# Kernel tuning notes

Hardware: AMD Instinct MI355X
Metric: run time of the kernel (lower is better)

Reference implementation:

```python
import jax, jax.numpy as jnp
import numpy as np

EPS = 1e-7
MAX_TANH = 1.0 - 1e-6  # clamp for arctanh stability


def _norm(v):
    # last-axis L2 norm, clamped away from zero
    return jnp.maximum(jnp.linalg.norm(v, axis=-1, keepdims=True), EPS)


def log_map_zero(y):
    # Poincare ball (c=1) log map at the origin
    n = _norm(y)
    return jnp.arctanh(jnp.clip(n, 0.0, MAX_TANH)) * y / n


def exp_map_zero(v):
    # Poincare ball (c=1) exp map at the origin
    n = _norm(v)
    return jnp.tanh(n) * v / n


def h_add(x, y):
    # Mobius addition x (+) y on the Poincare ball (c=1)
    xy = jnp.sum(x * y, axis=-1, keepdims=True)
    x2 = jnp.sum(x * x, axis=-1, keepdims=True)
    y2 = jnp.sum(y * y, axis=-1, keepdims=True)
    num = (1.0 + 2.0 * xy + y2) * x + (1.0 - x2) * y
    den = 1.0 + 2.0 * xy + x2 * y2
    return num / jnp.maximum(den, EPS)


def h_mul(x, W):
    # Mobius matrix-vector multiply: exp0( log0(x) @ W )
    return exp_map_zero(log_map_zero(x) @ W)


def setup_inputs() -> dict:
    key = jax.random.key(0)
    k1, k2, k3, k4 = jax.random.split(key, 4)
    N, F_IN, F_OUT = 8192, 128, 128
    # node features inside the unit ball: ||x|| ~ 0.05*sqrt(128) ~ 0.57
    x = 0.05 * jax.random.normal(k1, (N, F_IN), dtype=jnp.float32)
    # sparse-ish row-normalized dense adjacency
    a = (jax.random.uniform(k2, (N, N)) < 0.01).astype(jnp.float32)
    adj = a / jnp.maximum(a.sum(axis=1, keepdims=True), 1.0)
    # xavier-uniform-ish weights
    lim_e = np.sqrt(6.0 / (F_IN + F_IN)) * np.sqrt(2.0)
    lim_l = np.sqrt(6.0 / (2 * F_IN + F_OUT)) * np.sqrt(2.0)
    embed = jax.random.uniform(k3, (F_IN, F_IN), minval=-lim_e, maxval=lim_e, dtype=jnp.float32)
    layer = jax.random.uniform(k4, (2 * F_IN, F_OUT), minval=-lim_l, maxval=lim_l, dtype=jnp.float32)
    embed_bias = jnp.zeros((F_IN,), dtype=jnp.float32)
    layer_bias = jnp.zeros((F_OUT,), dtype=jnp.float32)
    return {"x": x, "adj": adj, "embed": embed, "layer": layer,
            "embed_bias": embed_bias, "layer_bias": layer_bias}


def reference(x, adj, embed, layer, embed_bias, layer_bias):
    # h = (embed (x)mobius x) (+) embed_bias
    h = h_mul(x, embed)                      # [N, F_IN]
    h = h_add(h, embed_bias[None, :])
    # neighbor aggregation in tangent space at origin
    neigh = exp_map_zero(adj @ log_map_zero(h))   # [N, F_IN]
    # out = (layer (x)mobius [x ; neigh]) (+) layer_bias
    out = h_mul(jnp.concatenate((x, neigh), axis=1), layer)  # [N, F_OUT]
    out = h_add(out, layer_bias[None, :])
    return out
```

## Files before the change

### kernel.cpp

```cpp
#include <hip/hip_runtime.h>
#include <hip/hip_bf16.h>
#include <math.h>

#define EPS  1e-7f
#define MAXT 0.999999f

typedef short  s16x8  __attribute__((ext_vector_type(8)));
typedef float  f32x16 __attribute__((ext_vector_type(16)));
typedef float  f32x4  __attribute__((ext_vector_type(4)));

__device__ __forceinline__ float waveRedSum(float v) {
    #pragma unroll
    for (int off = 32; off > 0; off >>= 1)
        v += __shfl_xor(v, off, 64);
    return v;
}

__device__ __forceinline__ unsigned short f2bf(float f) {
    unsigned u = __float_as_uint(f);
    u += 0x7fff + ((u >> 16) & 1);
    return (unsigned short)(u >> 16);
}

__global__ __launch_bounds__(256) void kA(const float* __restrict__ x,
                                          const float* __restrict__ embed,
                                          const float* __restrict__ ebias,
                                          unsigned short* __restrict__ vpack) {
    __shared__ float u[4][128];
    const int wave = threadIdx.x >> 6;
    const int lane = threadIdx.x & 63;
    const int row  = blockIdx.x * 4 + wave;
    const int c0   = lane * 2;

    const float2 xr = *(const float2*)(x + (size_t)row * 128 + c0);

    float n2 = waveRedSum(xr.x * xr.x + xr.y * xr.y);
    float n  = fmaxf(sqrtf(n2), EPS);
    float sc = atanhf(fminf(n, MAXT)) / n;
    u[wave][c0]     = xr.x * sc;
    u[wave][c0 + 1] = xr.y * sc;
    __syncthreads();

    float a0 = 0.f, a1 = 0.f;
    #pragma unroll 8
    for (int k = 0; k < 128; k++) {
        float  uk = u[wave][k];
        float2 e  = *(const float2*)(embed + (size_t)k * 128 + c0);
        a0 = fmaf(uk, e.x, a0);
        a1 = fmaf(uk, e.y, a1);
    }

    float np2 = waveRedSum(a0 * a0 + a1 * a1);
    float np  = fmaxf(sqrtf(np2), EPS);
    float se  = tanhf(np) / np;
    float h0 = a0 * se, h1 = a1 * se;
    float x2 = np2 * se * se;

    float bx = ebias[c0], by = ebias[c0 + 1];
    float xy = waveRedSum(h0 * bx + h1 * by);
    float y2 = waveRedSum(bx * bx + by * by);
    float den = fmaxf(1.f + 2.f * xy + x2 * y2, EPS);
    float cx = 1.f + 2.f * xy + y2;
    float cy = 1.f - x2;
    float hb0 = (cx * h0 + cy * bx) / den;
    float hb1 = (cx * h1 + cy * by) / den;

    float m2 = waveRedSum(hb0 * hb0 + hb1 * hb1);
    float m  = fmaxf(sqrtf(m2), EPS);
    float sl = atanhf(fminf(m, MAXT)) / m;
    float v0 = hb0 * sl, v1 = hb1 * sl;

    const int tbase = (row >> 4) * 2048 + (row & 15);
    vpack[tbase + c0 * 16]       = f2bf(v0);
    vpack[tbase + (c0 + 1) * 16] = f2bf(v1);
}

__device__ __forceinline__ s16x8 pack_bf16x8(const f32x4 a, const f32x4 b) {
    union { __hip_bfloat162 h[4]; s16x8 v; } r;
    r.h[0] = __float22bfloat162_rn({a.x, a.y});
    r.h[1] = __float22bfloat162_rn({a.z, a.w});
    r.h[2] = __float22bfloat162_rn({b.x, b.y});
    r.h[3] = __float22bfloat162_rn({b.z, b.w});
    return r.v;
}

__global__ __launch_bounds__(256) void kB(const float* __restrict__ adj,
                                          const unsigned short* __restrict__ vpack,
                                          float* __restrict__ tpart,
                                          int klen) {
    const int wave = threadIdx.x >> 6;
    const int lane = threadIdx.x & 63;
    const int rt   = blockIdx.x * 4 + wave;
    const int r0   = rt * 32;
    const int k0   = blockIdx.y * klen;
    float* tout    = tpart + (size_t)blockIdx.y * (8192 * 128);

    const int m  = lane & 31;
    const int kh = lane >> 5;

    const float* abase = adj + (size_t)(r0 + m) * 8192 + k0 + kh * 8;
    const unsigned short* bbase = vpack + (size_t)(k0 >> 4) * 2048 + m * 16 + kh * 8;

    const int kiters = klen >> 4;

    f32x16 acc0 = {0.f}, acc1 = {0.f}, acc2 = {0.f}, acc3 = {0.f};

    f32x4 aq[4][2];
    s16x8 bq[2][4];

    #pragma unroll
    for (int c = 0; c < 4; ++c) {
        aq[c][0] = *(const f32x4*)(abase + c * 16);
        aq[c][1] = *(const f32x4*)(abase + c * 16 + 4);
    }
    #pragma unroll
    for (int c = 0; c < 2; ++c) {
        const unsigned short* bp = bbase + (size_t)c * 2048;
        bq[c][0] = *(const s16x8*)(bp);
        bq[c][1] = *(const s16x8*)(bp + 512);
        bq[c][2] = *(const s16x8*)(bp + 1024);
        bq[c][3] = *(const s16x8*)(bp + 1536);
    }

    for (int it = 0; it < kiters; it += 4) {
        #pragma unroll
        for (int u = 0; u < 4; ++u) {
            const int c = it + u;
            s16x8 af = pack_bf16x8(aq[u][0], aq[u][1]);
            acc0 = __builtin_amdgcn_mfma_f32_32x32x16_bf16(af, bq[u & 1][0], acc0, 0, 0, 0);
            acc1 = __builtin_amdgcn_mfma_f32_32x32x16_bf16(af, bq[u & 1][1], acc1, 0, 0, 0);
            acc2 = __builtin_amdgcn_mfma_f32_32x32x16_bf16(af, bq[u & 1][2], acc2, 0, 0, 0);
            acc3 = __builtin_amdgcn_mfma_f32_32x32x16_bf16(af, bq[u & 1][3], acc3, 0, 0, 0);

            {
                const int cb = min(c + 2, kiters - 1);
                const unsigned short* bp = bbase + (size_t)cb * 2048;
                bq[u & 1][0] = *(const s16x8*)(bp);
                bq[u & 1][1] = *(const s16x8*)(bp + 512);
                bq[u & 1][2] = *(const s16x8*)(bp + 1024);
                bq[u & 1][3] = *(const s16x8*)(bp + 1536);
            }
            {
                const int ca = min(c + 4, kiters - 1);
                aq[u][0] = *(const f32x4*)(abase + (size_t)ca * 16);
                aq[u][1] = *(const f32x4*)(abase + (size_t)ca * 16 + 4);
            }
        }
    }

    #pragma unroll
    for (int r = 0; r < 16; ++r) {
        int row  = r0 + (r & 3) + 8 * (r >> 2) + 4 * kh;
        float* o = tout + (size_t)row * 128 + m;
        o[0]  = acc0[r];
        o[32] = acc1[r];
        o[64] = acc2[r];
        o[96] = acc3[r];
    }
}

__global__ __launch_bounds__(256) void kC(const float* __restrict__ x,
                                          const float* __restrict__ tpart,
                                          const float* __restrict__ layer,
                                          const float* __restrict__ lbias,
                                          float* __restrict__ out,
                                          int S) {
    __shared__ float w[4][256];
    const int wave = threadIdx.x >> 6;
    const int lane = threadIdx.x & 63;
    const int row  = blockIdx.x * 4 + wave;
    const int c0   = lane * 2;

    float2 tr = *(const float2*)(tpart + (size_t)row * 128 + c0);
    for (int s = 1; s < S; s++) {
        float2 p = *(const float2*)(tpart + (size_t)s * 8192 * 128 + (size_t)row * 128 + c0);
        tr.x += p.x; tr.y += p.y;
    }
    const float2 xr = *(const float2*)(x + (size_t)row * 128 + c0);

    float st = waveRedSum(tr.x * tr.x + tr.y * tr.y);
    float sx = waveRedSum(xr.x * xr.x + xr.y * xr.y);

    float nt = fmaxf(sqrtf(st), EPS);
    float se = tanhf(nt) / nt;

    float ncat2 = sx + st * se * se;
    float ncat  = fmaxf(sqrtf(ncat2), EPS);
    float sw    = atanhf(fminf(ncat, MAXT)) / ncat;
    w[wave][c0]           = xr.x * sw;
    w[wave][c0 + 1]       = xr.y * sw;
    w[wave][128 + c0]     = tr.x * se * sw;
    w[wave][128 + c0 + 1] = tr.y * se * sw;
    __syncthreads();

    float a0 = 0.f, a1 = 0.f;
    #pragma unroll 8
    for (int k = 0; k < 256; k++) {
        float  wk = w[wave][k];
        float2 e  = *(const float2*)(layer + (size_t)k * 128 + c0);
        a0 = fmaf(wk, e.x, a0);
        a1 = fmaf(wk, e.y, a1);
    }

    float np2 = waveRedSum(a0 * a0 + a1 * a1);
    float np  = fmaxf(sqrtf(np2), EPS);
    float so  = tanhf(np) / np;
    float o0 = a0 * so, o1 = a1 * so;
    float x2 = np2 * so * so;

    float bx = lbias[c0], by = lbias[c0 + 1];
    float xy = waveRedSum(o0 * bx + o1 * by);
    float y2 = waveRedSum(bx * bx + by * by);
    float den = fmaxf(1.f + 2.f * xy + x2 * y2, EPS);
    float cx = 1.f + 2.f * xy + y2;
    float cy = 1.f - x2;

    float2 res;
    res.x = (cx * o0 + cy * bx) / den;
    res.y = (cx * o1 + cy * by) / den;
    *(float2*)(out + (size_t)row * 128 + c0) = res;
}

extern "C" void kernel_launch(void* const* d_in, const int* in_sizes, int n_in,
                              void* d_out, int out_size, void* d_ws, size_t ws_size,
                              hipStream_t stream) {
    const float* x     = (const float*)d_in[0];
    const float* adj   = (const float*)d_in[1];
    const float* embed = (const float*)d_in[2];
    const float* layer = (const float*)d_in[3];
    const float* eb    = (const float*)d_in[4];
    const float* lb    = (const float*)d_in[5];
    float* out = (float*)d_out;

    const size_t vbytes = (size_t)8192 * 128 * 2;
    const size_t slice  = (size_t)8192 * 128 * 4;

    int S = 1;
    if      (ws_size >= vbytes + 8 * slice) S = 8;
    else if (ws_size >= vbytes + 4 * slice) S = 4;
    else if (ws_size >= vbytes + 2 * slice) S = 2;

    unsigned short* vpack = (unsigned short*)d_ws;
    float* tpart = (float*)((char*)d_ws + vbytes);

    kA<<<2048, 256, 0, stream>>>(x, embed, eb, vpack);
    kB<<<dim3(64, S), 256, 0, stream>>>(adj, vpack, tpart, 8192 / S);
    kC<<<2048, 256, 0, stream>>>(x, tpart, layer, lb, out, S);
}
```

Measured before the change: 530.3 us.

## Coalesce adjacency loads by row and transpose through per-wave LDS in kB

The adjacency-times-features GEMM kernel no longer has each lane read a 32-byte strip of its own row. Each wave now loads 2 rows x 128 columns per instruction, so a wave's 64 lanes read whole contiguous 512-byte row segments. It converts them to bf16 and writes them into a padded per-wave LDS tile, which is read back in the MFMA operand layout. This targets poorly coalesced global reads of the large adj matrix, which dominates the kernel's memory traffic. In exchange it adds LDS writes and reads, 16 live f32x4 registers of prefetch, and relies on wave-local ordering without explicit barriers. It also assumes klen is a multiple of 128.

```diff
diff --git a/kernel.cpp b/kernel.cpp
--- a/kernel.cpp
+++ b/kernel.cpp
@@ -75,19 +75,14 @@
     vpack[tbase + (c0 + 1) * 16] = f2bf(v1);
 }
 
-__device__ __forceinline__ s16x8 pack_bf16x8(const f32x4 a, const f32x4 b) {
-    union { __hip_bfloat162 h[4]; s16x8 v; } r;
-    r.h[0] = __float22bfloat162_rn({a.x, a.y});
-    r.h[1] = __float22bfloat162_rn({a.z, a.w});
-    r.h[2] = __float22bfloat162_rn({b.x, b.y});
-    r.h[3] = __float22bfloat162_rn({b.z, b.w});
-    return r.v;
-}
+#define KCPAD 1040
 
 __global__ __launch_bounds__(256) void kB(const float* __restrict__ adj,
                                           const unsigned short* __restrict__ vpack,
                                           float* __restrict__ tpart,
                                           int klen) {
+    __shared__ __align__(16) unsigned char lds[4][8 * KCPAD];
+
     const int wave = threadIdx.x >> 6;
     const int lane = threadIdx.x & 63;
     const int rt   = blockIdx.x * 4 + wave;
@@ -97,54 +92,66 @@
 
     const int m  = lane & 31;
     const int kh = lane >> 5;
-
-    const float* abase = adj + (size_t)(r0 + m) * 8192 + k0 + kh * 8;
-    const unsigned short* bbase = vpack + (size_t)(k0 >> 4) * 2048 + m * 16 + kh * 8;
-
-    const int kiters = klen >> 4;
+    unsigned char* buf = lds[wave];
+
+    const int lr = lane >> 5;
+    const int c0 = (lane & 31) * 4;
+    const float* aload = adj + (size_t)(r0 + lr) * 8192 + k0 + c0;
+    unsigned char* wbase = buf + (c0 >> 4) * KCPAD + lr * 32 + (c0 & 15) * 2;
+
+    const int g0 = k0 >> 4;
+    const int glast = (klen >> 4) - 1;
+    const unsigned short* bb = vpack + (size_t)m * 16 + kh * 8;
 
     f32x16 acc0 = {0.f}, acc1 = {0.f}, acc2 = {0.f}, acc3 = {0.f};
 
-    f32x4 aq[4][2];
+    f32x4 ar[16];
+    #pragma unroll
+    for (int j = 0; j < 16; ++j)
+        ar[j] = *(const f32x4*)(aload + (size_t)(2 * j) * 8192);
+
     s16x8 bq[2][4];
-
-    #pragma unroll
-    for (int c = 0; c < 4; ++c) {
-        aq[c][0] = *(const f32x4*)(abase + c * 16);
-        aq[c][1] = *(const f32x4*)(abase + c * 16 + 4);
-    }
     #pragma unroll
     for (int c = 0; c < 2; ++c) {
-        const unsigned short* bp = bbase + (size_t)c * 2048;
+        const unsigned short* bp = bb + (size_t)(g0 + c) * 2048;
         bq[c][0] = *(const s16x8*)(bp);
         bq[c][1] = *(const s16x8*)(bp + 512);
         bq[c][2] = *(const s16x8*)(bp + 1024);
         bq[c][3] = *(const s16x8*)(bp + 1536);
     }
 
-    for (int it = 0; it < kiters; it += 4) {
+    const int nsc = klen >> 7;
+    for (int sc = 0; sc < nsc; ++sc) {
         #pragma unroll
-        for (int u = 0; u < 4; ++u) {
-            const int c = it + u;
-            s16x8 af = pack_bf16x8(aq[u][0], aq[u][1]);
-            acc0 = __builtin_amdgcn_mfma_f32_32x32x16_bf16(af, bq[u & 1][0], acc0, 0, 0, 0);
-            acc1 = __builtin_amdgcn_mfma_f32_32x32x16_bf16(af, bq[u & 1][1], acc1, 0, 0, 0);
-            acc2 = __builtin_amdgcn_mfma_f32_32x32x16_bf16(af, bq[u & 1][2], acc2, 0, 0, 0);
-            acc3 = __builtin_amdgcn_mfma_f32_32x32x16_bf16(af, bq[u & 1][3], acc3, 0, 0, 0);
-
-            {
-                const int cb = min(c + 2, kiters - 1);
-                const unsigned short* bp = bbase + (size_t)cb * 2048;
-                bq[u & 1][0] = *(const s16x8*)(bp);
-                bq[u & 1][1] = *(const s16x8*)(bp + 512);
-                bq[u & 1][2] = *(const s16x8*)(bp + 1024);
-                bq[u & 1][3] = *(const s16x8*)(bp + 1536);
-            }
-            {
-                const int ca = min(c + 4, kiters - 1);
-                aq[u][0] = *(const f32x4*)(abase + (size_t)ca * 16);
-                aq[u][1] = *(const f32x4*)(abase + (size_t)ca * 16 + 4);
-            }
+        for (int j = 0; j < 16; ++j) {
+            union { __hip_bfloat162 h[2]; uint2 w; } p;
+            p.h[0] = __float22bfloat162_rn({ar[j].x, ar[j].y});
+            p.h[1] = __float22bfloat162_rn({ar[j].z, ar[j].w});
+            *(uint2*)(wbase + j * 64) = p.w;
+        }
+
+        if (sc + 1 < nsc) {
+            aload += 128;
+            #pragma unroll
+            for (int j = 0; j < 16; ++j)
+                ar[j] = *(const f32x4*)(aload + (size_t)(2 * j) * 8192);
+        }
+
+        #pragma unroll
+        for (int kc = 0; kc < 8; ++kc) {
+            const int g    = sc * 8 + kc;
+            const int slot = g & 1;
+            s16x8 a = *(const s16x8*)(buf + kc * KCPAD + m * 32 + kh * 16);
+            acc0 = __builtin_amdgcn_mfma_f32_32x32x16_bf16(a, bq[slot][0], acc0, 0, 0, 0);
+            acc1 = __builtin_amdgcn_mfma_f32_32x32x16_bf16(a, bq[slot][1], acc1, 0, 0, 0);
+            acc2 = __builtin_amdgcn_mfma_f32_32x32x16_bf16(a, bq[slot][2], acc2, 0, 0, 0);
+            acc3 = __builtin_amdgcn_mfma_f32_32x32x16_bf16(a, bq[slot][3], acc3, 0, 0, 0);
+            int gn = g + 2; if (gn > glast) gn = glast;
+            const unsigned short* bp = bb + (size_t)(g0 + gn) * 2048;
+            bq[slot][0] = *(const s16x8*)(bp);
+            bq[slot][1] = *(const s16x8*)(bp + 512);
+            bq[slot][2] = *(const s16x8*)(bp + 1024);
+            bq[slot][3] = *(const s16x8*)(bp + 1536);
         }
     }
 
```

Result: faster. 506.2 us (-4.5%).
